# Kernel tuning notes

Hardware: AMD Instinct MI355X
Metric: run time of the kernel (lower is better)

The kernel has to match this reference:

```python
import jax, jax.numpy as jnp
import numpy as np

DIM = 768
HEADS = 12
HEAD_DIM = DIM // HEADS
SCALE = HEAD_DIM ** -0.5


def setup_inputs() -> dict:
    key = jax.random.key(0)
    ks = jax.random.split(key, 6)
    B, N, C = 2, 2048, DIM
    x = jax.random.normal(ks[0], (B, N, C), dtype=jnp.float32)
    s = C ** -0.5
    Wq = jax.random.normal(ks[1], (C, C), dtype=jnp.float32) * s
    Wk = jax.random.normal(ks[2], (C, C), dtype=jnp.float32) * s
    Wv = jax.random.normal(ks[3], (C, C), dtype=jnp.float32) * s
    Wp = jax.random.normal(ks[4], (C, C), dtype=jnp.float32) * s
    bp = jax.random.normal(ks[5], (C,), dtype=jnp.float32) * 0.01
    return {"x": x, "Wq": Wq, "Wk": Wk, "Wv": Wv, "Wp": Wp, "bp": bp}


def reference(x, Wq, Wk, Wv, Wp, bp):
    B, N, C = x.shape
    h, d = HEADS, HEAD_DIM
    # projections (no bias), split heads: (B, h, N, d)
    Q = (x @ Wq.T).reshape(B, N, h, d).transpose(0, 2, 1, 3)
    K = (x @ Wk.T).reshape(B, N, h, d).transpose(0, 2, 1, 3)
    V = (x @ Wv.T).reshape(B, N, h, d).transpose(0, 2, 1, 3)
    # averaged key: (B, h, 1, d) -> scores (B, h, N)
    K_avg = K.mean(axis=2)  # (B, h, d)
    z = jnp.einsum('bhnd,bhd->bhn', Q, K_avg) * SCALE
    attn = jax.nn.softmax(z, axis=-1)  # (B, h, N)
    # circulant gather: roll[b,h,i,j] = attn[b,h,(j-i)%N] / N
    idx = (jnp.arange(N)[None, :] - jnp.arange(N)[:, None]) % N  # (N, N)
    roll = attn[:, :, idx] / N  # (B, h, N, N)
    out = jnp.einsum('bhij,bhjd->bhid', roll, V)  # (B, h, N, d)
    out = out.transpose(0, 2, 1, 3).reshape(B, N, C)
    return out @ Wp.T + bp
```

## Files before the change

### kernel.cpp

```cpp
#include <hip/hip_runtime.h>


typedef __bf16 bf16x8 __attribute__((ext_vector_type(8)));
typedef float  f32x4  __attribute__((ext_vector_type(4)));

#define AS_GLOBAL(p) ((const __attribute__((address_space(1))) unsigned int*)(p))
#define AS_LDS(p)    ((__attribute__((address_space(3))) unsigned int*)(p))

__device__ __forceinline__ void async16(const void* g, void* l) {
    __builtin_amdgcn_global_load_lds(AS_GLOBAL(g), AS_LDS(l), 16, 0, 0);
}

struct bf4 { __bf16 a, b, c, d; };

template <int BN, int MODE>
__device__ void gemm_phase(char* smem, const __bf16* __restrict__ A,
                           const __bf16* __restrict__ Bt, void* __restrict__ Cout,
                           const float* __restrict__ bias,
                           int K, int ldA, int ldBt, int ldC, int mBase, int nBase)
{
    constexpr int STRIDE = (128 + BN) * 32 * 2;
    constexpr int WN = BN / 2, NI = WN / 16;
    const int tid = threadIdx.x;
    const int lane = tid & 63, wid = tid >> 6;
    const int lane15 = lane & 15, quad = lane >> 4;
    const int wm = (wid & 1) * 64, wn = (wid >> 1) * WN;

    auto stage = [&](int kb, int buf) {
        __bf16* As = (__bf16*)(smem + buf * STRIDE);
        __bf16* Bs = As + 128 * 32;
#pragma unroll
        for (int c0 = 0; c0 < 512; c0 += 256) {
            int c = c0 + tid, row = c >> 2, slot = c & 3;
            int k8 = slot ^ ((row >> 1) & 3);
            async16(A + (size_t)(mBase + row) * ldA + kb + k8 * 8, As + c * 8);
        }
#pragma unroll
        for (int c0 = 0; c0 < BN * 4; c0 += 256) {
            int c = c0 + tid, row = c >> 2, slot = c & 3;
            int k8 = slot ^ ((row >> 1) & 3);
            async16(Bt + (size_t)(nBase + row) * ldBt + kb + k8 * 8, Bs + c * 8);
        }
    };

    f32x4 acc[4][NI] = {};
    const int nk = K >> 5;

    stage(0, 0);
    for (int ki = 0; ki < nk; ++ki) {
        __syncthreads();
        if (ki + 1 < nk) stage((ki + 1) << 5, (ki + 1) & 1);

        __bf16* As = (__bf16*)(smem + (ki & 1) * STRIDE);
        __bf16* Bs = As + 128 * 32;
        bf16x8 af[4], bv[NI];
#pragma unroll
        for (int mi = 0; mi < 4; ++mi) {
            int row = wm + mi * 16 + lane15;
            af[mi] = *(const bf16x8*)&As[row * 32 + (quad ^ ((row >> 1) & 3)) * 8];
        }
#pragma unroll
        for (int ni = 0; ni < NI; ++ni) {
            int row = wn + ni * 16 + lane15;
            bv[ni] = *(const bf16x8*)&Bs[row * 32 + (quad ^ ((row >> 1) & 3)) * 8];
        }
#pragma unroll
        for (int mi = 0; mi < 4; ++mi)
#pragma unroll
            for (int ni = 0; ni < NI; ++ni)
                acc[mi][ni] = __builtin_amdgcn_mfma_f32_16x16x32_bf16(
                    af[mi], bv[ni], acc[mi][ni], 0, 0, 0);
    }

#pragma unroll
    for (int mi = 0; mi < 4; ++mi)
#pragma unroll
        for (int ni = 0; ni < NI; ++ni)
#pragma unroll
            for (int r = 0; r < 4; ++r) {
                int row = mBase + wm + mi * 16 + quad * 4 + r;
                int col = nBase + wn + ni * 16 + lane15;
                float v = acc[mi][ni][r];
                if (MODE == 0) {
                    ((__bf16*)Cout)[(size_t)row * ldC + col] = (__bf16)v;
                } else if (MODE == 1) {
                    ((float*)Cout)[(size_t)row * ldC + col] = v + bias[col];
                } else {
                    int b = row >> 11;
                    if ((unsigned)(col - b * 12) < 12u)
                        ((float*)Cout)[(size_t)col * 2048 + (row & 2047)] = v;
                }
            }
}

__global__ __launch_bounds__(256)
void k_prep(const float* __restrict__ x, const float* __restrict__ Wv,
            const float* __restrict__ Wp,
            __bf16* __restrict__ xb, __bf16* __restrict__ Wvb,
            __bf16* __restrict__ Wpb, float* __restrict__ x_part)
{
    const int bid = blockIdx.x, tid = threadIdx.x;
    int idx = bid * 256 + tid;
    const float4* xf4 = (const float4*)x;
    bf4* xb4 = (bf4*)xb;
#pragma unroll
    for (int r = 0; r < 6; ++r) {
        float4 v = xf4[idx + r * 131072];
        xb4[idx + r * 131072] = bf4{(__bf16)v.x, (__bf16)v.y, (__bf16)v.z, (__bf16)v.w};
    }
    const float4* wv4 = (const float4*)Wv;  bf4* wvb4 = (bf4*)Wvb;
    const float4* wp4 = (const float4*)Wp;  bf4* wpb4 = (bf4*)Wpb;
#pragma unroll
    for (int r = 0; r < 2; ++r) {
        int i = idx + r * 131072;
        if (i < 147456) {
            float4 v = wv4[i];
            wvb4[i] = bf4{(__bf16)v.x, (__bf16)v.y, (__bf16)v.z, (__bf16)v.w};
            float4 w2 = wp4[i];
            wpb4[i] = bf4{(__bf16)w2.x, (__bf16)w2.y, (__bf16)w2.z, (__bf16)w2.w};
        }
    }
    if (bid < 96) {
        int c = (bid % 3) * 256 + tid;
        int gb = bid / 3, b = gb >> 4, g = gb & 15;
        const float* p = x + ((size_t)(b * 2048 + g * 128)) * 768 + c;
        float s = 0.f;
        for (int i2 = 0; i2 < 128; ++i2) s += p[(size_t)i2 * 768];
        x_part[(size_t)(b * 16 + g) * 768 + c] = s;
    }
}

__global__ __launch_bounds__(256)
void k_ub(const float* __restrict__ x_part, const float* __restrict__ Wk,
          const float* __restrict__ Wq, __bf16* __restrict__ Ub)
{
    const int bid = blockIdx.x, tid = threadIdx.x;
    if (bid >= 24) {
        for (int c = tid; c < 768; c += 256) Ub[(size_t)bid * 768 + c] = (__bf16)0.f;
        return;
    }
    __shared__ float sx[768];
    __shared__ float sk[64];
    int b = bid / 12, h = bid % 12;
    for (int c = tid; c < 768; c += 256) {
        float s = 0.f;
#pragma unroll
        for (int g = 0; g < 16; ++g)
            s += x_part[(size_t)(b * 16 + g) * 768 + c];
        sx[c] = s;
    }
    __syncthreads();
    {
        int d = tid >> 2, sub = tid & 3;
        const float* wk = Wk + (size_t)(h * 64 + d) * 768;
        float s = 0.f;
        for (int c = sub; c < 768; c += 4) s += sx[c] * wk[c];
        s += __shfl_down(s, 2);
        s += __shfl_down(s, 1);
        if (sub == 0) sk[d] = s * (0.125f / 2048.f);
    }
    __syncthreads();
    for (int c = tid; c < 768; c += 256) {
        float s = 0.f;
#pragma unroll 16
        for (int d2 = 0; d2 < 64; ++d2)
            s += sk[d2] * Wq[(size_t)(h * 64 + d2) * 768 + c];
        Ub[(size_t)bid * 768 + c] = (__bf16)s;
    }
}

__global__ __launch_bounds__(256, 2)
void k_gemms(const __bf16* __restrict__ xb, const __bf16* __restrict__ Wvb,
             const __bf16* __restrict__ Ub, __bf16* __restrict__ VT,
             float* __restrict__ z_t)
{
    __shared__ __attribute__((aligned(16))) char smem[32768];
    const int bid = blockIdx.x;
    if (bid < 192) {
        gemm_phase<128, 0>(smem, Wvb, xb, VT, nullptr, 768, 768, 768, 4096,
                           (bid / 32) * 128, (bid % 32) * 128);
    } else {
        gemm_phase<64, 2>(smem, xb, Ub, z_t, nullptr, 768, 768, 768, 0,
                          (bid - 192) * 128, 0);
    }
}

__global__ __launch_bounds__(256, 2)
void k_conv(const float* __restrict__ z_t, const __bf16* __restrict__ VT,
            __bf16* __restrict__ outp)
{
    __shared__ __attribute__((aligned(16))) char smem[53376];
    __bf16 (*rep)[2056] = (__bf16(*)[2056])smem;
    float* red = (float*)(smem + 32896);
    __bf16* attn_s = (__bf16*)(smem + 49280);

    const int bid = blockIdx.x, tid = threadIdx.x;
    const int lane = tid & 63, wid = tid >> 6;
    const int lane15 = lane & 15, quad = lane >> 4;
    const int bh = bid >> 4, b = bh / 12, h = bh % 12;
    const int m0 = (bid & 15) * 128 + (wid & 1) * 64;
    const int wn = (wid >> 1) * 32;

    {
        const float* z = z_t + (size_t)bh * 2048;
        float v[8];
        float m = -1e30f;
#pragma unroll
        for (int j = 0; j < 8; ++j) { v[j] = z[tid + j * 256]; m = fmaxf(m, v[j]); }
#pragma unroll
        for (int off = 32; off; off >>= 1) m = fmaxf(m, __shfl_xor(m, off));
        if (lane == 0) red[wid] = m;
        __syncthreads();
        m = fmaxf(fmaxf(red[0], red[1]), fmaxf(red[2], red[3]));
        __syncthreads();
        float s = 0.f;
#pragma unroll
        for (int j = 0; j < 8; ++j) { v[j] = __expf(v[j] - m); s += v[j]; }
#pragma unroll
        for (int off = 32; off; off >>= 1) s += __shfl_xor(s, off);
        if (lane == 0) red[wid] = s;
        __syncthreads();
        s = red[0] + red[1] + red[2] + red[3];
        float inv = 1.f / (s * 2048.f);
#pragma unroll
        for (int j = 0; j < 8; ++j)
            attn_s[tid + j * 256] = (__bf16)(v[j] * inv);
    }
    __syncthreads();
    for (int idx = tid; idx < 8 * 2048; idx += 256) {
        int a = idx >> 11, u = idx & 2047;
        rep[a][u] = attn_s[(u + a) & 2047];
    }

    const __bf16* vsrc = VT + (size_t)h * 64 * 4096 + b * 2048;

    auto stage = [&](int kb, int buf) {
        __bf16* vt = (__bf16*)(smem + 32896 + buf * 8192);
#pragma unroll
        for (int c0 = 0; c0 < 512; c0 += 256) {
            int c = c0 + tid, dd = c >> 3, slot = c & 7;
            int k8 = slot ^ (dd & 7);
            async16(vsrc + (size_t)dd * 4096 + kb * 64 + k8 * 8, vt + c * 8);
        }
    };

    f32x4 acc[4][2] = {};
    stage(0, 0);
    for (int kb = 0; kb < 32; ++kb) {
        __syncthreads();
        if (kb + 1 < 32) stage(kb + 1, (kb + 1) & 1);
        __bf16* vt = (__bf16*)(smem + 32896 + (kb & 1) * 8192);

#pragma unroll
        for (int ks = 0; ks < 2; ++ks) {
            int kloc = ks * 32 + quad * 8;
            int kglob = kb * 64 + kloc;
            bf16x8 af[4], bv[2];
#pragma unroll
            for (int mi = 0; mi < 4; ++mi) {
                int m = m0 + mi * 16 + lane15;
                int p = (kglob - m) & 2047;
                int al = p & 7;
                af[mi] = *(const bf16x8*)&rep[al][p - al];
            }
#pragma unroll
            for (int ni = 0; ni < 2; ++ni) {
                int dd = wn + ni * 16 + lane15;
                int slot = (kloc >> 3) ^ (dd & 7);
                bv[ni] = *(const bf16x8*)&vt[dd * 64 + slot * 8];
            }
#pragma unroll
            for (int mi = 0; mi < 4; ++mi)
#pragma unroll
                for (int ni = 0; ni < 2; ++ni)
                    acc[mi][ni] = __builtin_amdgcn_mfma_f32_16x16x32_bf16(
                        af[mi], bv[ni], acc[mi][ni], 0, 0, 0);
        }
    }

#pragma unroll
    for (int mi = 0; mi < 4; ++mi)
#pragma unroll
        for (int ni = 0; ni < 2; ++ni)
#pragma unroll
            for (int r = 0; r < 4; ++r) {
                int i = m0 + mi * 16 + quad * 4 + r;
                int dd = wn + ni * 16 + lane15;
                outp[(size_t)(b * 2048 + i) * 768 + h * 64 + dd] =
                    (__bf16)acc[mi][ni][r];
            }
}

__global__ __launch_bounds__(256, 2)
void k_out(const __bf16* __restrict__ out_pre, const __bf16* __restrict__ Wpb,
           const float* __restrict__ bp, float* __restrict__ out)
{
    __shared__ __attribute__((aligned(16))) char smem[32768];
    const int bid = blockIdx.x;
    gemm_phase<128, 1>(smem, out_pre, Wpb, out, bp, 768, 768, 768, 768,
                       (bid / 6) * 128, (bid % 6) * 128);
}

extern "C" void kernel_launch(void* const* d_in, const int* in_sizes, int n_in,
                              void* d_out, int out_size, void* d_ws, size_t ws_size,
                              hipStream_t stream)
{
    (void)in_sizes; (void)n_in; (void)out_size; (void)ws_size;
    const float* x  = (const float*)d_in[0];
    const float* Wq = (const float*)d_in[1];
    const float* Wk = (const float*)d_in[2];
    const float* Wv = (const float*)d_in[3];
    const float* Wp = (const float*)d_in[4];
    const float* bp = (const float*)d_in[5];

    char* w = (char*)d_ws;
    auto alloc = [&](size_t bytes) {
        char* p = w; w += (bytes + 255) & ~(size_t)255; return p;
    };
    float*  x_part  = (float*) alloc((size_t)32 * 768 * 4);
    __bf16* xb      = (__bf16*)alloc((size_t)4096 * 768 * 2);
    __bf16* Wvb     = (__bf16*)alloc((size_t)768 * 768 * 2);
    __bf16* Wpb     = (__bf16*)alloc((size_t)768 * 768 * 2);
    __bf16* Ub      = (__bf16*)alloc((size_t)64 * 768 * 2);
    float*  z_t     = (float*) alloc((size_t)24 * 2048 * 4);
    __bf16* VT      = (__bf16*)alloc((size_t)768 * 4096 * 2);
    __bf16* out_pre = (__bf16*)alloc((size_t)4096 * 768 * 2);

    k_prep <<<512, 256, 0, stream>>>(x, Wv, Wp, xb, Wvb, Wpb, x_part);
    k_ub   <<<64,  256, 0, stream>>>(x_part, Wk, Wq, Ub);
    k_gemms<<<224, 256, 0, stream>>>(xb, Wvb, Ub, VT, z_t);
    k_conv <<<384, 256, 0, stream>>>(z_t, VT, out_pre);
    k_out  <<<192, 256, 0, stream>>>(out_pre, Wpb, bp, (float*)d_out);
}
```

Measured before the change: 163.9 us.

## Fuse column sums into the conversion pass and widen conv tiles per block

Measured after the change: 169.6 us. +3.5%, slower.

```diff
diff --git a/kernel.cpp b/kernel.cpp
--- a/kernel.cpp
+++ b/kernel.cpp
@@ -97,67 +97,61 @@
 void k_prep(const float* __restrict__ x, const float* __restrict__ Wv,
             const float* __restrict__ Wp,
             __bf16* __restrict__ xb, __bf16* __restrict__ Wvb,
-            __bf16* __restrict__ Wpb, float* __restrict__ x_part)
+            __bf16* __restrict__ Wpb, float* __restrict__ x_avg)
 {
     const int bid = blockIdx.x, tid = threadIdx.x;
-    int idx = bid * 256 + tid;
-    const float4* xf4 = (const float4*)x;
-    bf4* xb4 = (bf4*)xb;
+    __shared__ float sums[768];
+    for (int c = tid; c < 768; c += 256) sums[c] = 0.f;
+    __syncthreads();
+
+    const float4* xs = (const float4*)x + (size_t)bid * 1536;
+    bf4* xd = (bf4*)xb + (size_t)bid * 1536;
 #pragma unroll
     for (int r = 0; r < 6; ++r) {
-        float4 v = xf4[idx + r * 131072];
-        xb4[idx + r * 131072] = bf4{(__bf16)v.x, (__bf16)v.y, (__bf16)v.z, (__bf16)v.w};
+        int j = tid + r * 256;
+        float4 v = xs[j];
+        xd[j] = bf4{(__bf16)v.x, (__bf16)v.y, (__bf16)v.z, (__bf16)v.w};
+        int col = (j % 192) * 4;
+        atomicAdd(&sums[col + 0], v.x);
+        atomicAdd(&sums[col + 1], v.y);
+        atomicAdd(&sums[col + 2], v.z);
+        atomicAdd(&sums[col + 3], v.w);
     }
     const float4* wv4 = (const float4*)Wv;  bf4* wvb4 = (bf4*)Wvb;
     const float4* wp4 = (const float4*)Wp;  bf4* wpb4 = (bf4*)Wpb;
-#pragma unroll
-    for (int r = 0; r < 2; ++r) {
-        int i = idx + r * 131072;
-        if (i < 147456) {
-            float4 v = wv4[i];
-            wvb4[i] = bf4{(__bf16)v.x, (__bf16)v.y, (__bf16)v.z, (__bf16)v.w};
-            float4 w2 = wp4[i];
-            wpb4[i] = bf4{(__bf16)w2.x, (__bf16)w2.y, (__bf16)w2.z, (__bf16)w2.w};
-        }
-    }
-    if (bid < 96) {
-        int c = (bid % 3) * 256 + tid;
-        int gb = bid / 3, b = gb >> 4, g = gb & 15;
-        const float* p = x + ((size_t)(b * 2048 + g * 128)) * 768 + c;
-        float s = 0.f;
-        for (int i2 = 0; i2 < 128; ++i2) s += p[(size_t)i2 * 768];
-        x_part[(size_t)(b * 16 + g) * 768 + c] = s;
-    }
+    for (int t = tid; t < 288; t += 256) {
+        int g = bid * 288 + t;
+        float4 v = wv4[g];
+        wvb4[g] = bf4{(__bf16)v.x, (__bf16)v.y, (__bf16)v.z, (__bf16)v.w};
+        float4 w2 = wp4[g];
+        wpb4[g] = bf4{(__bf16)w2.x, (__bf16)w2.y, (__bf16)w2.z, (__bf16)w2.w};
+    }
+    __syncthreads();
+    const int b = bid >> 8;
+    for (int c = tid; c < 768; c += 256)
+        atomicAdd(&x_avg[b * 768 + c], sums[c]);
 }
 
 __global__ __launch_bounds__(256)
-void k_ub(const float* __restrict__ x_part, const float* __restrict__ Wk,
+void k_ub(const float* __restrict__ x_avg, const float* __restrict__ Wk,
           const float* __restrict__ Wq, __bf16* __restrict__ Ub)
 {
     const int bid = blockIdx.x, tid = threadIdx.x;
-    if (bid >= 24) {
-        for (int c = tid; c < 768; c += 256) Ub[(size_t)bid * 768 + c] = (__bf16)0.f;
-        return;
-    }
+    const int lane = tid & 63, wid = tid >> 6;
     __shared__ float sx[768];
     __shared__ float sk[64];
     int b = bid / 12, h = bid % 12;
-    for (int c = tid; c < 768; c += 256) {
+    for (int c = tid; c < 768; c += 256) sx[c] = x_avg[b * 768 + c];
+    __syncthreads();
+    for (int round = 0; round < 16; ++round) {
+        int o = round * 4 + wid;
+        const float* wk = Wk + (size_t)(h * 64 + o) * 768;
         float s = 0.f;
 #pragma unroll
-        for (int g = 0; g < 16; ++g)
-            s += x_part[(size_t)(b * 16 + g) * 768 + c];
-        sx[c] = s;
-    }
-    __syncthreads();
-    {
-        int d = tid >> 2, sub = tid & 3;
-        const float* wk = Wk + (size_t)(h * 64 + d) * 768;
-        float s = 0.f;
-        for (int c = sub; c < 768; c += 4) s += sx[c] * wk[c];
-        s += __shfl_down(s, 2);
-        s += __shfl_down(s, 1);
-        if (sub == 0) sk[d] = s * (0.125f / 2048.f);
+        for (int cc0 = 0; cc0 < 768; cc0 += 64) s += sx[cc0 + lane] * wk[cc0 + lane];
+#pragma unroll
+        for (int off = 32; off; off >>= 1) s += __shfl_down(s, off);
+        if (lane == 0) sk[o] = s * (0.125f / 2048.f);
     }
     __syncthreads();
     for (int c = tid; c < 768; c += 256) {
@@ -197,9 +191,8 @@
     const int bid = blockIdx.x, tid = threadIdx.x;
     const int lane = tid & 63, wid = tid >> 6;
     const int lane15 = lane & 15, quad = lane >> 4;
-    const int bh = bid >> 4, b = bh / 12, h = bh % 12;
-    const int m0 = (bid & 15) * 128 + (wid & 1) * 64;
-    const int wn = (wid >> 1) * 32;
+    const int bh = bid >> 3, b = bh / 12, h = bh % 12;
+    const int m0 = (bid & 7) * 256 + wid * 64;
 
     {
         const float* z = z_t + (size_t)bh * 2048;
@@ -244,7 +237,7 @@
         }
     };
 
-    f32x4 acc[4][2] = {};
+    f32x4 acc[4][4] = {};
     stage(0, 0);
     for (int kb = 0; kb < 32; ++kb) {
         __syncthreads();
@@ -255,7 +248,7 @@
         for (int ks = 0; ks < 2; ++ks) {
             int kloc = ks * 32 + quad * 8;
             int kglob = kb * 64 + kloc;
-            bf16x8 af[4], bv[2];
+            bf16x8 af[4], bv[4];
 #pragma unroll
             for (int mi = 0; mi < 4; ++mi) {
                 int m = m0 + mi * 16 + lane15;
@@ -264,15 +257,15 @@
                 af[mi] = *(const bf16x8*)&rep[al][p - al];
             }
 #pragma unroll
-            for (int ni = 0; ni < 2; ++ni) {
-                int dd = wn + ni * 16 + lane15;
+            for (int ni = 0; ni < 4; ++ni) {
+                int dd = ni * 16 + lane15;
                 int slot = (kloc >> 3) ^ (dd & 7);
                 bv[ni] = *(const bf16x8*)&vt[dd * 64 + slot * 8];
             }
 #pragma unroll
             for (int mi = 0; mi < 4; ++mi)
 #pragma unroll
-                for (int ni = 0; ni < 2; ++ni)
+                for (int ni = 0; ni < 4; ++ni)
                     acc[mi][ni] = __builtin_amdgcn_mfma_f32_16x16x32_bf16(
                         af[mi], bv[ni], acc[mi][ni], 0, 0, 0);
         }
@@ -281,11 +274,11 @@
 #pragma unroll
     for (int mi = 0; mi < 4; ++mi)
 #pragma unroll
-        for (int ni = 0; ni < 2; ++ni)
+        for (int ni = 0; ni < 4; ++ni)
 #pragma unroll
             for (int r = 0; r < 4; ++r) {
                 int i = m0 + mi * 16 + quad * 4 + r;
-                int dd = wn + ni * 16 + lane15;
+                int dd = ni * 16 + lane15;
                 outp[(size_t)(b * 2048 + i) * 768 + h * 64 + dd] =
                     (__bf16)acc[mi][ni][r];
             }
@@ -317,7 +310,7 @@
     auto alloc = [&](size_t bytes) {
         char* p = w; w += (bytes + 255) & ~(size_t)255; return p;
     };
-    float*  x_part  = (float*) alloc((size_t)32 * 768 * 4);
+    float*  x_avg   = (float*) alloc((size_t)2 * 768 * 4);
     __bf16* xb      = (__bf16*)alloc((size_t)4096 * 768 * 2);
     __bf16* Wvb     = (__bf16*)alloc((size_t)768 * 768 * 2);
     __bf16* Wpb     = (__bf16*)alloc((size_t)768 * 768 * 2);
@@ -326,9 +319,10 @@
     __bf16* VT      = (__bf16*)alloc((size_t)768 * 4096 * 2);
     __bf16* out_pre = (__bf16*)alloc((size_t)4096 * 768 * 2);
 
-    k_prep <<<512, 256, 0, stream>>>(x, Wv, Wp, xb, Wvb, Wpb, x_part);
-    k_ub   <<<64,  256, 0, stream>>>(x_part, Wk, Wq, Ub);
+    hipMemsetAsync(x_avg, 0, 2 * 768 * sizeof(float), stream);
+    k_prep <<<512, 256, 0, stream>>>(x, Wv, Wp, xb, Wvb, Wpb, x_avg);
+    k_ub   <<<24,  256, 0, stream>>>(x_avg, Wk, Wq, Ub);
     k_gemms<<<224, 256, 0, stream>>>(xb, Wvb, Ub, VT, z_t);
-    k_conv <<<384, 256, 0, stream>>>(z_t, VT, out_pre);
+    k_conv <<<192, 256, 0, stream>>>(z_t, VT, out_pre);
     k_out  <<<192, 256, 0, stream>>>(out_pre, Wpb, bp, (float*)d_out);
 }
```
